# Kernel optimization log

Measured on AMD Instinct MI355X. Metric: run time of the kernel, lower is better.

The kernel has to match this reference:

```python
import jax, jax.numpy as jnp
import numpy as np

# RNN-T joint network: broadcast encoder (B,T,D) and decoder (B,U,D) states,
# concat on feature dim -> (B,T,U,2D), then Linear(2D -> C, bias=False).
# Mathematically identical efficient form: split W = [W_enc | W_dec] along its
# input dim and compute two small GEMMs + broadcast add, avoiding the (B,T,U,2D)
# intermediate. cat(e,d) @ W^T == e @ W_enc^T + d @ W_dec^T.

B, T, U, D, C = 4, 256, 64, 512, 1024


def setup_inputs() -> dict:
    key = jax.random.key(0)
    k1, k2, k3 = jax.random.split(key, 3)
    encoder_outputs = jax.random.normal(k1, (B, T, D), dtype=jnp.float32)
    decoder_outputs = jax.random.normal(k2, (B, U, D), dtype=jnp.float32)
    # fc weight: (num_classes, 2*encoder_dim), torch Linear layout
    W = jax.random.normal(k3, (C, 2 * D), dtype=jnp.float32) * (1.0 / np.sqrt(2 * D))
    return {"encoder_outputs": encoder_outputs, "decoder_outputs": decoder_outputs, "W": W}


def reference(encoder_outputs, decoder_outputs, W):
    d = encoder_outputs.shape[-1]
    W_enc, W_dec = W[:, :d], W[:, d:]
    # (B,T,C) and (B,U,C), then broadcast add -> (B,T,U,C)
    enc_proj = jnp.einsum("btd,cd->btc", encoder_outputs, W_enc)
    dec_proj = jnp.einsum("bud,cd->buc", decoder_outputs, W_dec)
    return enc_proj[:, :, None, :] + dec_proj[:, None, :, :]
```

## Files before the change

kernel.cpp:

```cpp
#include <hip/hip_runtime.h>
#include <hip/hip_bf16.h>


typedef float v4f   __attribute__((ext_vector_type(4)));
typedef float f32x4 __attribute__((ext_vector_type(4)));
typedef __attribute__((ext_vector_type(8))) short short8;

__device__ inline short bf16_of(float f) {
    __hip_bfloat16 h = __float2bfloat16(f);
    return *reinterpret_cast<short*>(&h);
}

__global__ __launch_bounds__(256) void cvt_frag(
    const float* __restrict__ enc, const float* __restrict__ dec,
    const float* __restrict__ W,
    ushort* __restrict__ Xe_f, ushort* __restrict__ Xd_f,
    ushort* __restrict__ We_f, ushort* __restrict__ Wd_f)
{
    const int tid  = threadIdx.x;
    const int lane = tid & 63;
    const int l16  = lane & 15;
    const int kq   = lane >> 4;
    const int gid  = blockIdx.x * 4 + (tid >> 6);

    const float* src; ushort* dst; int g, rs, co;
    if (gid < 1024)      { src = enc; dst = Xe_f; g = gid;        rs = 512;  co = 0;   }
    else if (gid < 1280) { src = dec; dst = Xd_f; g = gid - 1024; rs = 512;  co = 0;   }
    else if (gid < 2304) { src = W;   dst = We_f; g = gid - 1280; rs = 1024; co = 0;   }
    else                 { src = W;   dst = Wd_f; g = gid - 2304; rs = 1024; co = 512; }

    const int rb = g >> 4, kbi = g & 15;
    const float* p = src + (size_t)(rb * 16 + l16) * rs + co + kbi * 32 + kq * 8;
    float4 lo = *(const float4*)p;
    float4 hi = *(const float4*)(p + 4);
    short8 o;
    o[0] = bf16_of(lo.x); o[1] = bf16_of(lo.y); o[2] = bf16_of(lo.z); o[3] = bf16_of(lo.w);
    o[4] = bf16_of(hi.x); o[5] = bf16_of(hi.y); o[6] = bf16_of(hi.z); o[7] = bf16_of(hi.w);
    *(short8*)&dst[(size_t)g * 512 + lane * 8] = o;
}

__global__ __launch_bounds__(256) void dec_gemm_bf16(
    const ushort* __restrict__ Xd_f, const ushort* __restrict__ Wd_f,
    float* __restrict__ Pd)
{
    const int tid  = threadIdx.x;
    const int wave = tid >> 6;
    const int lane = tid & 63;
    const int l16  = lane & 15;
    const int kq   = lane >> 4;

    const int kz = wave >> 1;
    const int wn = (wave & 1) * 32;
    const int mb = blockIdx.y;
    const int cBase = blockIdx.x * 64;
    const int cb0 = blockIdx.x * 4 + (wave & 1) * 2;

    const short8* xa  = (const short8*)Xd_f + (size_t)(mb  * 16 + kz * 8) * 64 + lane;
    const short8* wb0 = (const short8*)Wd_f + (size_t)(cb0       * 16 + kz * 8) * 64 + lane;
    const short8* wb1 = (const short8*)Wd_f + (size_t)((cb0 + 1) * 16 + kz * 8) * 64 + lane;

    f32x4 a0 = {0.f,0.f,0.f,0.f}, a1 = {0.f,0.f,0.f,0.f};
#pragma unroll
    for (int s = 0; s < 8; ++s) {
        short8 a  = xa [(size_t)s * 64];
        short8 b0 = wb0[(size_t)s * 64];
        short8 b1 = wb1[(size_t)s * 64];
        a0 = __builtin_amdgcn_mfma_f32_16x16x32_bf16(a, b0, a0, 0, 0, 0);
        a1 = __builtin_amdgcn_mfma_f32_16x16x32_bf16(a, b1, a1, 0, 0, 0);
    }

    __shared__ float Ps[16][65];
    if (kz == 1) {
#pragma unroll
        for (int r = 0; r < 4; ++r) {
            Ps[kq * 4 + r][wn + l16]      = a0[r];
            Ps[kq * 4 + r][wn + 16 + l16] = a1[r];
        }
    }
    __syncthreads();
    if (kz == 0) {
        float* p0 = Pd + (size_t)(mb * 16) * 1024 + cBase + wn;
#pragma unroll
        for (int r = 0; r < 4; ++r) {
            const int row = kq * 4 + r;
            p0[(size_t)row * 1024 + l16]      = a0[r] + Ps[row][wn + l16];
            p0[(size_t)row * 1024 + 16 + l16] = a1[r] + Ps[row][wn + 16 + l16];
        }
    }
}

__global__ __launch_bounds__(256) void fused_enc_stream(
    const ushort* __restrict__ Xe_f, const ushort* __restrict__ We_f,
    const float* __restrict__ Pd, float* __restrict__ out)
{
    const int tid  = threadIdx.x;
    const int wave = tid >> 6;
    const int lane = tid & 63;
    const int l16  = lane & 15;
    const int kq   = lane >> 4;

    const int kz = wave >> 1;
    const int wn = (wave & 1) * 32;
    const int btBase = blockIdx.y * 16;
    const int cBase  = blockIdx.x * 64;
    const int b      = blockIdx.y >> 4;
    const int cb0    = blockIdx.x * 4 + (wave & 1) * 2;

    __shared__ float encS[2][16][68];
    __shared__ float decS[64][64];

#pragma unroll
    for (int p = 0; p < 4; ++p) {
        int s    = tid + p * 256;
        int row  = s >> 4;
        int slot = s & 15;
        float4 v = *(const float4*)&Pd[(size_t)(b * 64 + row) * 1024 + cBase + slot * 4];
        *(float4*)&decS[row][slot * 4] = v;
    }

    {
        const short8* xa  = (const short8*)Xe_f + (size_t)(blockIdx.y * 16 + kz * 8) * 64 + lane;
        const short8* wb0 = (const short8*)We_f + (size_t)(cb0       * 16 + kz * 8) * 64 + lane;
        const short8* wb1 = (const short8*)We_f + (size_t)((cb0 + 1) * 16 + kz * 8) * 64 + lane;
        f32x4 a0 = {0.f,0.f,0.f,0.f}, a1 = {0.f,0.f,0.f,0.f};
#pragma unroll
        for (int s = 0; s < 8; ++s) {
            short8 a  = xa [(size_t)s * 64];
            short8 b0 = wb0[(size_t)s * 64];
            short8 b1 = wb1[(size_t)s * 64];
            a0 = __builtin_amdgcn_mfma_f32_16x16x32_bf16(a, b0, a0, 0, 0, 0);
            a1 = __builtin_amdgcn_mfma_f32_16x16x32_bf16(a, b1, a1, 0, 0, 0);
        }
#pragma unroll
        for (int r = 0; r < 4; ++r) {
            encS[kz][kq * 4 + r][wn + l16]      = a0[r];
            encS[kz][kq * 4 + r][wn + 16 + l16] = a1[r];
        }
    }

    __syncthreads();

    const int row = tid >> 4;
    const int c4  = (tid & 15) * 4;

    const float4 e0 = *(const float4*)&encS[0][row][c4];
    const float4 e1 = *(const float4*)&encS[1][row][c4];
    const v4f e = {e0.x + e1.x, e0.y + e1.y, e0.z + e1.z, e0.w + e1.w};

    float* po = out + (size_t)(btBase + row) * 64 * 1024 + cBase + c4;

#pragma unroll 8
    for (int u = 0; u < 64; ++u) {
        float4 d = *(const float4*)&decS[u][c4];
        v4f r = {e.x + d.x, e.y + d.y, e.z + d.z, e.w + d.w};
        *(v4f*)&po[(size_t)u * 1024] = r;
    }
}

extern "C" void kernel_launch(void* const* d_in, const int* in_sizes, int n_in,
                              void* d_out, int out_size, void* d_ws, size_t ws_size,
                              hipStream_t stream) {
    const float* enc = (const float*)d_in[0];
    const float* dec = (const float*)d_in[1];
    const float* W   = (const float*)d_in[2];
    float* out = (float*)d_out;

    char* ws = (char*)d_ws;
    float*  Pd   = (float*)(ws);
    ushort* Xe_f = (ushort*)(ws + (1u << 20));
    ushort* Xd_f = (ushort*)(ws + (2u << 20));
    ushort* We_f = (ushort*)(ws + (2u << 20) + (1u << 18));
    ushort* Wd_f = (ushort*)(ws + (3u << 20) + (1u << 18));

    cvt_frag<<<dim3(832), 256, 0, stream>>>(enc, dec, W, Xe_f, Xd_f, We_f, Wd_f);
    dec_gemm_bf16<<<dim3(16, 16), 256, 0, stream>>>(Xd_f, Wd_f, Pd);
    fused_enc_stream<<<dim3(16, 64), 256, 0, stream>>>(Xe_f, We_f, Pd, out);
}
```

Before: 55.99 us.

## Fuse decoder GEMM into conversion kernel and stream Pd directly from global

Merges the bf16 conversion and the decoder projection GEMM into one launch. Extra blocks convert dec and W_dec on the fly from fp32, so the Xd/Wd fragment buffers are no longer built. The encoder-stream kernel also stops staging the decoder projection tile in shared memory and reads Pd straight from global (L2) inside the output loop. This removes a kernel launch and some shared-memory traffic, at the cost of uncoalesced strided fp32 loads in the dec GEMM and more global reads per output row.

```diff
diff --git a/kernel.cpp b/kernel.cpp
--- a/kernel.cpp
+++ b/kernel.cpp
@@ -11,60 +11,58 @@
     return *reinterpret_cast<short*>(&h);
 }
 
-__global__ __launch_bounds__(256) void cvt_frag(
-    const float* __restrict__ enc, const float* __restrict__ dec,
-    const float* __restrict__ W,
-    ushort* __restrict__ Xe_f, ushort* __restrict__ Xd_f,
-    ushort* __restrict__ We_f, ushort* __restrict__ Wd_f)
-{
-    const int tid  = threadIdx.x;
-    const int lane = tid & 63;
-    const int l16  = lane & 15;
-    const int kq   = lane >> 4;
-    const int gid  = blockIdx.x * 4 + (tid >> 6);
-
-    const float* src; ushort* dst; int g, rs, co;
-    if (gid < 1024)      { src = enc; dst = Xe_f; g = gid;        rs = 512;  co = 0;   }
-    else if (gid < 1280) { src = dec; dst = Xd_f; g = gid - 1024; rs = 512;  co = 0;   }
-    else if (gid < 2304) { src = W;   dst = We_f; g = gid - 1280; rs = 1024; co = 0;   }
-    else                 { src = W;   dst = Wd_f; g = gid - 2304; rs = 1024; co = 512; }
-
-    const int rb = g >> 4, kbi = g & 15;
-    const float* p = src + (size_t)(rb * 16 + l16) * rs + co + kbi * 32 + kq * 8;
+__device__ inline short8 load_cvt_bf16x8(const float* __restrict__ p) {
     float4 lo = *(const float4*)p;
     float4 hi = *(const float4*)(p + 4);
-    short8 o;
-    o[0] = bf16_of(lo.x); o[1] = bf16_of(lo.y); o[2] = bf16_of(lo.z); o[3] = bf16_of(lo.w);
-    o[4] = bf16_of(hi.x); o[5] = bf16_of(hi.y); o[6] = bf16_of(hi.z); o[7] = bf16_of(hi.w);
-    *(short8*)&dst[(size_t)g * 512 + lane * 8] = o;
+    short8 r;
+    r[0] = bf16_of(lo.x); r[1] = bf16_of(lo.y); r[2] = bf16_of(lo.z); r[3] = bf16_of(lo.w);
+    r[4] = bf16_of(hi.x); r[5] = bf16_of(hi.y); r[6] = bf16_of(hi.z); r[7] = bf16_of(hi.w);
+    return r;
 }
 
-__global__ __launch_bounds__(256) void dec_gemm_bf16(
-    const ushort* __restrict__ Xd_f, const ushort* __restrict__ Wd_f,
+__global__ __launch_bounds__(256) void cvt_and_dec(
+    const float* __restrict__ enc,
+    const float* __restrict__ dec,
+    const float* __restrict__ W,
+    ushort* __restrict__ Xe_f, ushort* __restrict__ We_f,
     float* __restrict__ Pd)
 {
     const int tid  = threadIdx.x;
-    const int wave = tid >> 6;
+    const int w    = tid >> 6;
     const int lane = tid & 63;
     const int l16  = lane & 15;
     const int kq   = lane >> 4;
 
-    const int kz = wave >> 1;
-    const int wn = (wave & 1) * 32;
-    const int mb = blockIdx.y;
-    const int cBase = blockIdx.x * 64;
-    const int cb0 = blockIdx.x * 4 + (wave & 1) * 2;
+    if (blockIdx.x < 512) {
+        const int gid = blockIdx.x * 4 + w;
+        const float* src; ushort* dst; int g, rs;
+        if (gid < 1024) { src = enc; dst = Xe_f; g = gid;        rs = 512;  }
+        else            { src = W;   dst = We_f; g = gid - 1024; rs = 1024; }
+        const int rb = g >> 4, kbi = g & 15;
+        const float* p = src + (size_t)(rb * 16 + l16) * rs + kbi * 32 + kq * 8;
+        short8 o = load_cvt_bf16x8(p);
+        *(short8*)&dst[(size_t)g * 512 + lane * 8] = o;
+        return;
+    }
 
-    const short8* xa  = (const short8*)Xd_f + (size_t)(mb  * 16 + kz * 8) * 64 + lane;
-    const short8* wb0 = (const short8*)Wd_f + (size_t)(cb0       * 16 + kz * 8) * 64 + lane;
-    const short8* wb1 = (const short8*)Wd_f + (size_t)((cb0 + 1) * 16 + kz * 8) * 64 + lane;
+    const int task  = blockIdx.x - 512;
+    const int mb    = task >> 4;
+    const int cb4   = task & 15;
+    const int kz    = w >> 1;
+    const int wn    = (w & 1) * 32;
+    const int cBase = cb4 * 64;
+
+    const float* xr  = dec + (size_t)(mb * 16 + l16) * 512 + kz * 256;
+    const float* wr0 = W + (size_t)(cBase + wn + l16) * 1024 + 512 + kz * 256;
+    const float* wr1 = wr0 + (size_t)16 * 1024;
 
     f32x4 a0 = {0.f,0.f,0.f,0.f}, a1 = {0.f,0.f,0.f,0.f};
-#pragma unroll
-    for (int s = 0; s < 8; ++s) {
-        short8 a  = xa [(size_t)s * 64];
-        short8 b0 = wb0[(size_t)s * 64];
-        short8 b1 = wb1[(size_t)s * 64];
+#pragma unroll 4
+    for (int kb = 0; kb < 256; kb += 32) {
+        const int k = kb + kq * 8;
+        short8 a  = load_cvt_bf16x8(xr + k);
+        short8 b0 = load_cvt_bf16x8(wr0 + k);
+        short8 b1 = load_cvt_bf16x8(wr1 + k);
         a0 = __builtin_amdgcn_mfma_f32_16x16x32_bf16(a, b0, a0, 0, 0, 0);
         a1 = __builtin_amdgcn_mfma_f32_16x16x32_bf16(a, b1, a1, 0, 0, 0);
     }
@@ -90,8 +88,10 @@
 }
 
 __global__ __launch_bounds__(256) void fused_enc_stream(
-    const ushort* __restrict__ Xe_f, const ushort* __restrict__ We_f,
-    const float* __restrict__ Pd, float* __restrict__ out)
+    const ushort* __restrict__ Xe_f,
+    const ushort* __restrict__ We_f,
+    const float* __restrict__ Pd,
+    float* __restrict__ out)
 {
     const int tid  = threadIdx.x;
     const int wave = tid >> 6;
@@ -107,16 +107,6 @@
     const int cb0    = blockIdx.x * 4 + (wave & 1) * 2;
 
     __shared__ float encS[2][16][68];
-    __shared__ float decS[64][64];
-
-#pragma unroll
-    for (int p = 0; p < 4; ++p) {
-        int s    = tid + p * 256;
-        int row  = s >> 4;
-        int slot = s & 15;
-        float4 v = *(const float4*)&Pd[(size_t)(b * 64 + row) * 1024 + cBase + slot * 4];
-        *(float4*)&decS[row][slot * 4] = v;
-    }
 
     {
         const short8* xa  = (const short8*)Xe_f + (size_t)(blockIdx.y * 16 + kz * 8) * 64 + lane;
@@ -147,11 +137,12 @@
     const float4 e1 = *(const float4*)&encS[1][row][c4];
     const v4f e = {e0.x + e1.x, e0.y + e1.y, e0.z + e1.z, e0.w + e1.w};
 
-    float* po = out + (size_t)(btBase + row) * 64 * 1024 + cBase + c4;
+    const float* pd = Pd + (size_t)(b * 64) * 1024 + cBase + c4;
+    float*       po = out + (size_t)(btBase + row) * 64 * 1024 + cBase + c4;
 
 #pragma unroll 8
     for (int u = 0; u < 64; ++u) {
-        float4 d = *(const float4*)&decS[u][c4];
+        float4 d = *(const float4*)&pd[(size_t)u * 1024];
         v4f r = {e.x + d.x, e.y + d.y, e.z + d.z, e.w + d.w};
         *(v4f*)&po[(size_t)u * 1024] = r;
     }
@@ -168,11 +159,8 @@
     char* ws = (char*)d_ws;
     float*  Pd   = (float*)(ws);
     ushort* Xe_f = (ushort*)(ws + (1u << 20));
-    ushort* Xd_f = (ushort*)(ws + (2u << 20));
-    ushort* We_f = (ushort*)(ws + (2u << 20) + (1u << 18));
-    ushort* Wd_f = (ushort*)(ws + (3u << 20) + (1u << 18));
+    ushort* We_f = (ushort*)(ws + (2u << 20));
 
-    cvt_frag<<<dim3(832), 256, 0, stream>>>(enc, dec, W, Xe_f, Xd_f, We_f, Wd_f);
-    dec_gemm_bf16<<<dim3(16, 16), 256, 0, stream>>>(Xd_f, Wd_f, Pd);
+    cvt_and_dec<<<dim3(768), 256, 0, stream>>>(enc, dec, W, Xe_f, We_f, Pd);
     fused_enc_stream<<<dim3(16, 64), 256, 0, stream>>>(Xe_f, We_f, Pd, out);
 }
```

Result: slower. 57.67 us (+3.0%).

## Widen fused enc-stream blocks to 1024 threads and read dec proj from global

Applied to the files above, without the earlier changes.

The fused kernel now uses 1024-thread blocks, each covering 256 output columns instead of 64. Every wave computes one 16x16 encoder tile over the full K, so the split-K partial reduction is gone. The decoder projection is read straight from global memory (L2) in the broadcast-add loop instead of being staged in shared memory. This cuts shared-memory traffic and block count, but now depends on L2 hits for Pd and uses fewer, larger blocks (256 total), which may lower occupancy.

```diff
diff --git a/kernel.cpp b/kernel.cpp
--- a/kernel.cpp
+++ b/kernel.cpp
@@ -89,69 +89,50 @@
     }
 }
 
-__global__ __launch_bounds__(256) void fused_enc_stream(
-    const ushort* __restrict__ Xe_f, const ushort* __restrict__ We_f,
-    const float* __restrict__ Pd, float* __restrict__ out)
+__global__ __launch_bounds__(1024) void fused_enc_stream(
+    const ushort* __restrict__ Xe_f,
+    const ushort* __restrict__ We_f,
+    const float* __restrict__ Pd,
+    float* __restrict__ out)
 {
     const int tid  = threadIdx.x;
-    const int wave = tid >> 6;
+    const int w    = tid >> 6;
     const int lane = tid & 63;
     const int l16  = lane & 15;
     const int kq   = lane >> 4;
 
-    const int kz = wave >> 1;
-    const int wn = (wave & 1) * 32;
     const int btBase = blockIdx.y * 16;
-    const int cBase  = blockIdx.x * 64;
+    const int cBase  = blockIdx.x * 256;
     const int b      = blockIdx.y >> 4;
-    const int cb0    = blockIdx.x * 4 + (wave & 1) * 2;
+    const int cb     = blockIdx.x * 16 + w;
 
-    __shared__ float encS[2][16][68];
-    __shared__ float decS[64][64];
-
-#pragma unroll
-    for (int p = 0; p < 4; ++p) {
-        int s    = tid + p * 256;
-        int row  = s >> 4;
-        int slot = s & 15;
-        float4 v = *(const float4*)&Pd[(size_t)(b * 64 + row) * 1024 + cBase + slot * 4];
-        *(float4*)&decS[row][slot * 4] = v;
-    }
+    __shared__ float encS[16][260];
 
     {
-        const short8* xa  = (const short8*)Xe_f + (size_t)(blockIdx.y * 16 + kz * 8) * 64 + lane;
-        const short8* wb0 = (const short8*)We_f + (size_t)(cb0       * 16 + kz * 8) * 64 + lane;
-        const short8* wb1 = (const short8*)We_f + (size_t)((cb0 + 1) * 16 + kz * 8) * 64 + lane;
-        f32x4 a0 = {0.f,0.f,0.f,0.f}, a1 = {0.f,0.f,0.f,0.f};
+        const short8* xa = (const short8*)Xe_f + (size_t)(blockIdx.y * 16) * 64 + lane;
+        const short8* wb = (const short8*)We_f + (size_t)(cb * 16) * 64 + lane;
+        f32x4 acc = {0.f, 0.f, 0.f, 0.f};
 #pragma unroll
-        for (int s = 0; s < 8; ++s) {
-            short8 a  = xa [(size_t)s * 64];
-            short8 b0 = wb0[(size_t)s * 64];
-            short8 b1 = wb1[(size_t)s * 64];
-            a0 = __builtin_amdgcn_mfma_f32_16x16x32_bf16(a, b0, a0, 0, 0, 0);
-            a1 = __builtin_amdgcn_mfma_f32_16x16x32_bf16(a, b1, a1, 0, 0, 0);
+        for (int s = 0; s < 16; ++s) {
+            short8 a  = xa[(size_t)s * 64];
+            short8 bf = wb[(size_t)s * 64];
+            acc = __builtin_amdgcn_mfma_f32_16x16x32_bf16(a, bf, acc, 0, 0, 0);
         }
 #pragma unroll
-        for (int r = 0; r < 4; ++r) {
-            encS[kz][kq * 4 + r][wn + l16]      = a0[r];
-            encS[kz][kq * 4 + r][wn + 16 + l16] = a1[r];
-        }
+        for (int r = 0; r < 4; ++r)
+            encS[kq * 4 + r][w * 16 + l16] = acc[r];
     }
 
     __syncthreads();
 
-    const int row = tid >> 4;
-    const int c4  = (tid & 15) * 4;
+    const float4 e = *(const float4*)&encS[w][lane * 4];
 
-    const float4 e0 = *(const float4*)&encS[0][row][c4];
-    const float4 e1 = *(const float4*)&encS[1][row][c4];
-    const v4f e = {e0.x + e1.x, e0.y + e1.y, e0.z + e1.z, e0.w + e1.w};
-
-    float* po = out + (size_t)(btBase + row) * 64 * 1024 + cBase + c4;
+    const float* pd = Pd + (size_t)(b * 64) * 1024 + cBase + lane * 4;
+    float*       po = out + ((size_t)(btBase + w) * 64) * 1024 + cBase + lane * 4;
 
 #pragma unroll 8
     for (int u = 0; u < 64; ++u) {
-        float4 d = *(const float4*)&decS[u][c4];
+        float4 d = *(const float4*)&pd[(size_t)u * 1024];
         v4f r = {e.x + d.x, e.y + d.y, e.z + d.z, e.w + d.w};
         *(v4f*)&po[(size_t)u * 1024] = r;
     }
@@ -174,5 +155,5 @@
 
     cvt_frag<<<dim3(832), 256, 0, stream>>>(enc, dec, W, Xe_f, Xd_f, We_f, Wd_f);
     dec_gemm_bf16<<<dim3(16, 16), 256, 0, stream>>>(Xd_f, Wd_f, Pd);
-    fused_enc_stream<<<dim3(16, 64), 256, 0, stream>>>(Xe_f, We_f, Pd, out);
+    fused_enc_stream<<<dim3(4, 64), 1024, 0, stream>>>(Xe_f, We_f, Pd, out);
 }
```

Result: slower. 58.69 us (+4.8%).
